# Performance work log

Measured on AMD Instinct MI355X. Metric: run time of the kernel, lower is better.

Reference implementation:

```python
import jax, jax.numpy as jnp
import numpy as np

N = 100000   # nodes
E = 1600000  # edges (avg degree 16)
D = 128      # in = hidden = out channels
DROP_P = 0.2


def setup_inputs() -> dict:
    key = jax.random.key(0)
    ks = jax.random.split(key, 11)
    s = 1.0 / np.sqrt(D)  # glorot-ish scale
    inp = {
        "features": jax.random.normal(ks[0], (N, D), jnp.float32),
        "edge_index": jax.random.randint(ks[1], (2, E), 0, N, dtype=jnp.int64),
    }
    for i in range(3):
        inp[f"Wl{i}"] = jax.random.normal(ks[2 + 3 * i], (D, D), jnp.float32) * s
        inp[f"Wr{i}"] = jax.random.normal(ks[3 + 3 * i], (D, D), jnp.float32) * s
        inp[f"b{i}"] = jnp.zeros((D,), jnp.float32)
    return inp


def _sage_conv(x, src, dst, Wl, Wr, b):
    # PyG SAGEConv (aggr='max'): out = lin_l(max_{j->i} x_j) + lin_r(x_i)
    agg = jax.ops.segment_max(x[src], dst, num_segments=N)  # [N, D_in]
    agg = jnp.where(jnp.isfinite(agg), agg, 0.0)  # isolated nodes -> 0 (torch_scatter zero-init)
    return agg @ Wl + x @ Wr + b


def _dropout(x, key, p=DROP_P):
    keep = jax.random.bernoulli(key, 1.0 - p, x.shape)
    return jnp.where(keep, x / (1.0 - p), 0.0)


def reference(features, edge_index, Wl0, Wr0, b0, Wl1, Wr1, b1, Wl2, Wr2, b2):
    src, dst = edge_index[0], edge_index[1]
    k1, k2 = jax.random.split(jax.random.key(42))
    x = _sage_conv(features, src, dst, Wl0, Wr0, b0)
    x = _dropout(jax.nn.elu(x), k1)
    x = _sage_conv(x, src, dst, Wl1, Wr1, b1)
    x = _dropout(jax.nn.elu(x), k2)
    x = _sage_conv(x, src, dst, Wl2, Wr2, b2)
    return x
```

## Files before the change

kernel.cpp:

```cpp
#include <hip/hip_runtime.h>
#include <math.h>

#define D 128
#define BSHIFT 9
#define BCAP 12288

typedef __attribute__((ext_vector_type(8))) _Float16 half8;
typedef __attribute__((ext_vector_type(4))) float floatx4;

__host__ __device__ __forceinline__ unsigned rotl32(unsigned v, int r) {
  return (v << r) | (v >> (32 - r));
}

__host__ __device__ __forceinline__ void threefry2x32(unsigned k0, unsigned k1,
                                                      unsigned x0, unsigned x1,
                                                      unsigned &o0, unsigned &o1) {
  unsigned ks2 = k0 ^ k1 ^ 0x1BD11BDAu;
  unsigned v0 = x0 + k0;
  unsigned v1 = x1 + k1;
  v0 += v1; v1 = rotl32(v1, 13); v1 ^= v0;
  v0 += v1; v1 = rotl32(v1, 15); v1 ^= v0;
  v0 += v1; v1 = rotl32(v1, 26); v1 ^= v0;
  v0 += v1; v1 = rotl32(v1, 6);  v1 ^= v0;
  v0 += k1; v1 += ks2 + 1u;
  v0 += v1; v1 = rotl32(v1, 17); v1 ^= v0;
  v0 += v1; v1 = rotl32(v1, 29); v1 ^= v0;
  v0 += v1; v1 = rotl32(v1, 16); v1 ^= v0;
  v0 += v1; v1 = rotl32(v1, 24); v1 ^= v0;
  v0 += ks2; v1 += k0 + 2u;
  v0 += v1; v1 = rotl32(v1, 13); v1 ^= v0;
  v0 += v1; v1 = rotl32(v1, 15); v1 ^= v0;
  v0 += v1; v1 = rotl32(v1, 26); v1 ^= v0;
  v0 += v1; v1 = rotl32(v1, 6);  v1 ^= v0;
  v0 += k0; v1 += k1 + 3u;
  v0 += v1; v1 = rotl32(v1, 17); v1 ^= v0;
  v0 += v1; v1 = rotl32(v1, 29); v1 ^= v0;
  v0 += v1; v1 = rotl32(v1, 16); v1 ^= v0;
  v0 += v1; v1 = rotl32(v1, 24); v1 ^= v0;
  v0 += k1; v1 += ks2 + 4u;
  v0 += v1; v1 = rotl32(v1, 13); v1 ^= v0;
  v0 += v1; v1 = rotl32(v1, 15); v1 ^= v0;
  v0 += v1; v1 = rotl32(v1, 26); v1 ^= v0;
  v0 += v1; v1 = rotl32(v1, 6);  v1 ^= v0;
  v0 += ks2; v1 += k0 + 5u;
  o0 = v0; o1 = v1;
}

__device__ __forceinline__ unsigned short f2h(float f) {
  _Float16 h = (_Float16)f;
  return *(unsigned short*)&h;
}

__device__ __forceinline__ unsigned pkmax(unsigned a, unsigned b) {
  unsigned r;
  asm("v_pk_max_f16 %0, %1, %2" : "=v"(r) : "v"(a), "v"(b));
  return r;
}


__global__ __launch_bounds__(256) void bucket_count_kernel(
    const int* __restrict__ dst, int* __restrict__ bucketTotal, int nEdges) {
  __shared__ int lc[256];
  int t = threadIdx.x;
  lc[t] = 0;
  __syncthreads();
  int e0 = blockIdx.x * 4096;
  for (int i = t; i < 4096; i += 256) {
    int e = e0 + i;
    if (e < nEdges) atomicAdd(&lc[dst[e] >> BSHIFT], 1);
  }
  __syncthreads();
  int c = lc[t];
  if (c > 0) atomicAdd(&bucketTotal[t], c);
}

__global__ __launch_bounds__(256) void scan_buckets_kernel(
    const int* __restrict__ bucketTotal, int* __restrict__ buckOff,
    int* __restrict__ bucketCursor, int nBuck) {
  __shared__ int s[256];
  int t = threadIdx.x;
  int v = (t < nBuck) ? bucketTotal[t] : 0;
  s[t] = v;
  __syncthreads();
  for (int off = 1; off < 256; off <<= 1) {
    int u = (t >= off) ? s[t - off] : 0;
    __syncthreads();
    s[t] += u;
    __syncthreads();
  }
  int excl = s[t] - v;
  if (t < nBuck) {
    buckOff[t] = excl;
    bucketCursor[t] = excl;
  } else if (t == nBuck) {
    buckOff[t] = s[255];
  }
}

__global__ __launch_bounds__(256) void bucket_scatter_kernel(
    const int* __restrict__ src, const int* __restrict__ dst,
    int* __restrict__ bucketCursor, unsigned* __restrict__ pairs,
    int nEdges, int nBuck) {
  __shared__ int lcount[256];
  __shared__ int lbase[256];
  __shared__ int loff[256];
  int t = threadIdx.x;
  lcount[t] = 0; loff[t] = 0;
  __syncthreads();
  int e0 = blockIdx.x * 4096;
  for (int i = t; i < 4096; i += 256) {
    int e = e0 + i;
    if (e < nEdges) atomicAdd(&lcount[dst[e] >> BSHIFT], 1);
  }
  __syncthreads();
  if (t < nBuck) {
    int c = lcount[t];
    if (c > 0) lbase[t] = atomicAdd(&bucketCursor[t], c);
  }
  __syncthreads();
  for (int i = t; i < 4096; i += 256) {
    int e = e0 + i;
    if (e < nEdges) {
      int d = dst[e];
      int b = d >> BSHIFT;
      int lp = atomicAdd(&loff[b], 1);
      pairs[lbase[b] + lp] = ((unsigned)src[e] << BSHIFT) | ((unsigned)d & 511u);
    }
  }
}

__global__ __launch_bounds__(256) void local_fill_kernel(
    const unsigned* __restrict__ pairs, const int* __restrict__ buckOff,
    int* __restrict__ rowStart, int* __restrict__ csrSrc,
    int nNodes, int nBuck) {
  __shared__ int sData[BCAP];
  __shared__ int lcnt[1 << BSHIFT];
  __shared__ int sSum[256];
  int b = blockIdx.x;
  int node0 = b << BSHIFT;
  int base = buckOff[b];
  int end = buckOff[b + 1];
  int cnt = end - base;
  int t = threadIdx.x;

  lcnt[t] = 0;
  lcnt[t + 256] = 0;
  __syncthreads();

  for (int i = base + t; i < end; i += 256)
    atomicAdd(&lcnt[pairs[i] & 511u], 1);
  __syncthreads();

  int c0 = lcnt[2 * t];
  int c1 = lcnt[2 * t + 1];
  int local = c0 + c1;
  sSum[t] = local;
  __syncthreads();
  for (int off = 1; off < 256; off <<= 1) {
    int v = (t >= off) ? sSum[t - off] : 0;
    __syncthreads();
    sSum[t] += v;
    __syncthreads();
  }
  int excl = sSum[t] - local;
  __syncthreads();
  lcnt[2 * t] = excl;
  lcnt[2 * t + 1] = excl + c0;
  int n0 = node0 + 2 * t;
  int n1 = n0 + 1;
  if (n0 < nNodes) rowStart[n0] = base + excl;
  if (n1 < nNodes) rowStart[n1] = base + excl + c0;
  if (b == nBuck - 1 && t == 255) rowStart[nNodes] = end;
  __syncthreads();

  if (cnt <= BCAP) {
    for (int i = base + t; i < end; i += 256) {
      unsigned p = pairs[i];
      int lp = atomicAdd(&lcnt[p & 511u], 1);
      sData[lp] = (int)(p >> BSHIFT);
    }
    __syncthreads();
    for (int i = t; i < cnt; i += 256)
      csrSrc[base + i] = sData[i];
  } else {
    for (int i = base + t; i < end; i += 256) {
      unsigned p = pairs[i];
      int lp = atomicAdd(&lcnt[p & 511u], 1);
      csrSrc[base + lp] = (int)(p >> BSHIFT);
    }
  }
}

__global__ __launch_bounds__(256) void convert_feat_kernel(
    const float* __restrict__ f, unsigned short* __restrict__ o, int nElems) {
  int i = (blockIdx.x * 256 + threadIdx.x) * 4;
  if (i + 3 < nElems) {
    float4 v = *((const float4*)(f + i));
    unsigned a = (unsigned)f2h(v.x) | ((unsigned)f2h(v.y) << 16);
    unsigned b = (unsigned)f2h(v.z) | ((unsigned)f2h(v.w) << 16);
    *((uint2*)(o + i)) = make_uint2(a, b);
  } else {
    for (int j = i; j < nElems; ++j) o[j] = f2h(f[j]);
  }
}

__global__ __launch_bounds__(256) void pack_weights_kernel(
    const float* __restrict__ Wl0, const float* __restrict__ Wr0,
    const float* __restrict__ Wl1, const float* __restrict__ Wr1,
    const float* __restrict__ Wl2, const float* __restrict__ Wr2,
    unsigned short* __restrict__ Wt) {
  int t = blockIdx.x * 256 + threadIdx.x;
  if (t >= 3 * 128 * 256) return;
  int l = t >> 15;
  int rem = t & 32767;
  int n = rem >> 8;
  int k = rem & 255;
  const float* Wl = (l == 0) ? Wl0 : (l == 1) ? Wl1 : Wl2;
  const float* Wr = (l == 0) ? Wr0 : (l == 1) ? Wr1 : Wr2;
  float v = (k < 128) ? Wl[k * D + n] : Wr[(k - 128) * D + n];
  Wt[t] = f2h(v);
}

__global__ __launch_bounds__(256) void gather_max_f16_kernel(
    const uint4* __restrict__ x8, const int* __restrict__ rowStart,
    const int* __restrict__ csrSrc, uint4* __restrict__ agg8, int nNodes) {
  int n = blockIdx.x * 4 + (threadIdx.x >> 6);
  if (n >= nNodes) return;
  int lane = threadIdx.x & 63;
  int q = lane >> 4;
  int l16 = lane & 15;
  int e0 = rowStart[n], e1 = rowStart[n + 1];
  unsigned m0 = 0xFC00FC00u, m1 = 0xFC00FC00u,
           m2 = 0xFC00FC00u, m3 = 0xFC00FC00u;
  int e = e0;
  for (; e + 15 < e1; e += 16) {
    int sa = csrSrc[e + q];
    int sb = csrSrc[e + 4 + q];
    int sc = csrSrc[e + 8 + q];
    int sd = csrSrc[e + 12 + q];
    uint4 va = x8[(size_t)sa * 16 + l16];
    uint4 vb = x8[(size_t)sb * 16 + l16];
    uint4 vc = x8[(size_t)sc * 16 + l16];
    uint4 vd = x8[(size_t)sd * 16 + l16];
    m0 = pkmax(m0, pkmax(pkmax(va.x, vb.x), pkmax(vc.x, vd.x)));
    m1 = pkmax(m1, pkmax(pkmax(va.y, vb.y), pkmax(vc.y, vd.y)));
    m2 = pkmax(m2, pkmax(pkmax(va.z, vb.z), pkmax(vc.z, vd.z)));
    m3 = pkmax(m3, pkmax(pkmax(va.w, vb.w), pkmax(vc.w, vd.w)));
  }
  if (e + 7 < e1) {
    int sa = csrSrc[e + q];
    int sb = csrSrc[e + 4 + q];
    uint4 va = x8[(size_t)sa * 16 + l16];
    uint4 vb = x8[(size_t)sb * 16 + l16];
    m0 = pkmax(m0, pkmax(va.x, vb.x));
    m1 = pkmax(m1, pkmax(va.y, vb.y));
    m2 = pkmax(m2, pkmax(va.z, vb.z));
    m3 = pkmax(m3, pkmax(va.w, vb.w));
    e += 8;
  }
  if (e + 3 < e1) {
    int sa = csrSrc[e + q];
    uint4 va = x8[(size_t)sa * 16 + l16];
    m0 = pkmax(m0, va.x); m1 = pkmax(m1, va.y);
    m2 = pkmax(m2, va.z); m3 = pkmax(m3, va.w);
    e += 4;
  }
  for (; e < e1; ++e) {
    int sa = csrSrc[e];
    uint4 va = x8[(size_t)sa * 16 + l16];
    m0 = pkmax(m0, va.x); m1 = pkmax(m1, va.y);
    m2 = pkmax(m2, va.z); m3 = pkmax(m3, va.w);
  }
  m0 = pkmax(m0, (unsigned)__shfl_xor((int)m0, 16, 64));
  m1 = pkmax(m1, (unsigned)__shfl_xor((int)m1, 16, 64));
  m2 = pkmax(m2, (unsigned)__shfl_xor((int)m2, 16, 64));
  m3 = pkmax(m3, (unsigned)__shfl_xor((int)m3, 16, 64));
  m0 = pkmax(m0, (unsigned)__shfl_xor((int)m0, 32, 64));
  m1 = pkmax(m1, (unsigned)__shfl_xor((int)m1, 32, 64));
  m2 = pkmax(m2, (unsigned)__shfl_xor((int)m2, 32, 64));
  m3 = pkmax(m3, (unsigned)__shfl_xor((int)m3, 32, 64));
  uint4 r = make_uint4(0u, 0u, 0u, 0u);
  if (e0 != e1) r = make_uint4(m0, m1, m2, m3);
  if (q == 0) agg8[(size_t)n * 16 + l16] = r;
}

#define PA 280
#define TROWS 64

__global__ __launch_bounds__(256, 2) void fused_mfma_kernel(
    const unsigned short* __restrict__ agghf, unsigned short* __restrict__ xhf,
    const unsigned short* __restrict__ Wt, const float* __restrict__ bias,
    float* __restrict__ outF, int nRows, int mode, unsigned kk0, unsigned kk1) {
  __shared__ unsigned short sA[TROWS * PA];

  const int tid = threadIdx.x;
  const int row0 = blockIdx.x * TROWS;
  const int wv = tid >> 6, lane = tid & 63;
  const int quad = lane >> 4, m16 = lane & 15;
  const int nbase = wv * 32;

#pragma unroll
  for (int i = 0; i < 8; ++i) {
    int idx = i * 256 + tid;
    int r = idx >> 5;
    int seg = idx & 31;
    uint4 v = make_uint4(0, 0, 0, 0);
    if (row0 + r < nRows) {
      if (seg < 16) v = ((const uint4*)(agghf + (size_t)(row0 + r) * D))[seg];
      else          v = ((const uint4*)(xhf  + (size_t)(row0 + r) * D))[seg - 16];
    }
    *((uint4*)(sA + r * PA + seg * 8)) = v;
  }

  half8 bfr[2][4][2];
#pragma unroll
  for (int kc = 0; kc < 2; ++kc)
#pragma unroll
    for (int ks = 0; ks < 4; ++ks)
#pragma unroll
      for (int j = 0; j < 2; ++j)
        bfr[kc][ks][j] = *((const half8*)(
            Wt + (size_t)(nbase + j * 16 + m16) * 256 + kc * 128 + ks * 32 + quad * 8));

  unsigned dmask = 0u;
  if (mode < 2) {
#pragma unroll
    for (int j = 0; j < 2; ++j) {
      int col = nbase + j * 16 + m16;
#pragma unroll
      for (int i = 0; i < 4; ++i) {
#pragma unroll
        for (int reg = 0; reg < 4; ++reg) {
          int r = row0 + i * 16 + quad * 4 + reg;
          unsigned jj = (unsigned)r * D + col;
          unsigned y0, y1;
          threefry2x32(kk0, kk1, 0u, jj, y0, y1);
          float u = __uint_as_float((((y0 ^ y1) >> 9)) | 0x3F800000u) - 1.0f;
          if (u < 0.8f) dmask |= (1u << (j * 16 + i * 4 + reg));
        }
      }
    }
  }

  floatx4 acc[4][2];
#pragma unroll
  for (int i = 0; i < 4; ++i)
#pragma unroll
    for (int j = 0; j < 2; ++j) acc[i][j] = (floatx4)(0.0f);

  __syncthreads();

#pragma unroll
  for (int kc = 0; kc < 2; ++kc)
#pragma unroll
    for (int ks = 0; ks < 4; ++ks) {
      int kA = kc * 128 + ks * 32 + quad * 8;
#pragma unroll
      for (int i = 0; i < 4; ++i) {
        half8 a = *((const half8*)(sA + (m16 + 16 * i) * PA + kA));
        acc[i][0] = __builtin_amdgcn_mfma_f32_16x16x32_f16(a, bfr[kc][ks][0], acc[i][0], 0, 0, 0);
        acc[i][1] = __builtin_amdgcn_mfma_f32_16x16x32_f16(a, bfr[kc][ks][1], acc[i][1], 0, 0, 0);
      }
    }

  if (mode < 2) {
    __syncthreads();
#pragma unroll
    for (int j = 0; j < 2; ++j) {
      int col = nbase + j * 16 + m16;
      float bc = bias[col];
#pragma unroll
      for (int i = 0; i < 4; ++i) {
#pragma unroll
        for (int reg = 0; reg < 4; ++reg) {
          int r = i * 16 + quad * 4 + reg;
          if (row0 + r >= nRows) continue;
          float v = acc[i][j][reg] + bc;
          v = (v > 0.0f) ? v : (__expf(v) - 1.0f);
          v = ((dmask >> (j * 16 + i * 4 + reg)) & 1u) ? v * 1.25f : 0.0f;
          sA[r * PA + col] = f2h(v);
        }
      }
    }
    __syncthreads();
#pragma unroll
    for (int i = 0; i < 4; ++i) {
      int idx = i * 256 + tid;
      int r = idx >> 4;
      int seg = idx & 15;
      if (row0 + r < nRows)
        ((uint4*)xhf)[(size_t)(row0 + r) * 16 + seg] =
            *((const uint4*)(sA + r * PA + seg * 8));
    }
  } else {
#pragma unroll
    for (int j = 0; j < 2; ++j) {
      int col = nbase + j * 16 + m16;
      float bc = bias[col];
#pragma unroll
      for (int i = 0; i < 4; ++i) {
#pragma unroll
        for (int reg = 0; reg < 4; ++reg) {
          int r = row0 + i * 16 + quad * 4 + reg;
          if (r >= nRows) continue;
          outF[(size_t)r * D + col] = acc[i][j][reg] + bc;
        }
      }
    }
  }
}

extern "C" void kernel_launch(void* const* d_in, const int* in_sizes, int n_in,
                              void* d_out, int out_size, void* d_ws, size_t ws_size,
                              hipStream_t stream) {
  const float* feat = (const float*)d_in[0];
  const int* ei = (const int*)d_in[1];
  const float* Wl0 = (const float*)d_in[2];
  const float* Wr0 = (const float*)d_in[3];
  const float* b0 = (const float*)d_in[4];
  const float* Wl1 = (const float*)d_in[5];
  const float* Wr1 = (const float*)d_in[6];
  const float* b1 = (const float*)d_in[7];
  const float* Wl2 = (const float*)d_in[8];
  const float* Wr2 = (const float*)d_in[9];
  const float* b2 = (const float*)d_in[10];

  const int N = in_sizes[0] / D;
  const int E = in_sizes[1] / 2;
  const int* src = ei;
  const int* dst = ei + E;

  const size_t hfBytes = (size_t)N * D * 2;
  char* wsp = (char*)d_ws;
  size_t off = 0;
  unsigned short* xhf   = (unsigned short*)(wsp + off); off += hfBytes;
  unsigned short* agghf = (unsigned short*)(wsp + off); off += hfBytes;
  unsigned short* Wt    = (unsigned short*)(wsp + off); off += ((size_t)3 * 128 * 256 * 2 + 511) & ~511ull;
  int* rowStart     = (int*)(wsp + off); off += ((size_t)(N + 1) * 4 + 511) & ~511ull;
  int* bucketTotal  = (int*)(wsp + off); off += 2048;
  int* buckOff      = (int*)(wsp + off); off += 2048;
  int* bucketCursor = (int*)(wsp + off); off += 2048;
  int* csrSrc    = (int*)(wsp + off); off += (size_t)E * 4;
  unsigned* pairs = (unsigned*)(wsp + off); off += (size_t)E * 4;

  const int nBuck = (N + (1 << BSHIFT) - 1) >> BSHIFT;

  unsigned k1a, k1b, k2a, k2b;
  threefry2x32(0u, 42u, 0u, 0u, k1a, k1b);
  threefry2x32(0u, 42u, 0u, 1u, k2a, k2b);

  hipMemsetAsync(bucketTotal, 0, 1024, stream);
  bucket_count_kernel<<<(E + 4095) / 4096, 256, 0, stream>>>(dst, bucketTotal, E);
  scan_buckets_kernel<<<1, 256, 0, stream>>>(bucketTotal, buckOff, bucketCursor, nBuck);
  bucket_scatter_kernel<<<(E + 4095) / 4096, 256, 0, stream>>>(src, dst, bucketCursor, pairs, E, nBuck);
  local_fill_kernel<<<nBuck, 256, 0, stream>>>(pairs, buckOff, rowStart, csrSrc, N, nBuck);

  convert_feat_kernel<<<(N * D / 4 + 255) / 256, 256, 0, stream>>>(feat, xhf, N * D);
  pack_weights_kernel<<<(3 * 128 * 256 + 255) / 256, 256, 0, stream>>>(
      Wl0, Wr0, Wl1, Wr1, Wl2, Wr2, Wt);

  dim3 blk(256);
  dim3 grdMax((N + 3) / 4);
  dim3 grdGemm((N + TROWS - 1) / TROWS);
  float* outF = (float*)d_out;

  gather_max_f16_kernel<<<grdMax, blk, 0, stream>>>((const uint4*)xhf, rowStart, csrSrc, (uint4*)agghf, N);
  fused_mfma_kernel<<<grdGemm, blk, 0, stream>>>(agghf, xhf, Wt, b0, outF, N, 0, k1a, k1b);

  gather_max_f16_kernel<<<grdMax, blk, 0, stream>>>((const uint4*)xhf, rowStart, csrSrc, (uint4*)agghf, N);
  fused_mfma_kernel<<<grdGemm, blk, 0, stream>>>(agghf, xhf, Wt + 32768, b1, outF, N, 1, k2a, k2b);

  gather_max_f16_kernel<<<grdMax, blk, 0, stream>>>((const uint4*)xhf, rowStart, csrSrc, (uint4*)agghf, N);
  fused_mfma_kernel<<<grdGemm, blk, 0, stream>>>(agghf, xhf, Wt + 65536, b2, outF, N, 2, 0u, 0u);
}
```

Measured before the change: 483.3 us.

## Merge prep kernels into one launch and shrink GEMM tile to 48 rows

Feature conversion, weight packing and bucket counting now run as block ranges of a single prep kernel, which removes two launches and lets these independent jobs overlap. The fused MFMA kernel drops from 64 to 48 rows per block, with launch bounds raised to 5 blocks per CU, so each block uses less LDS and more blocks stay resident to hide the latency of staging and the epilogue. In exchange each block reloads the same weight fragments over fewer rows, and the dropout mask bit packing is reindexed to match the smaller tile.

```diff
diff --git a/kernel.cpp b/kernel.cpp
--- a/kernel.cpp
+++ b/kernel.cpp
@@ -57,21 +57,51 @@
   return r;
 }
 
-
-__global__ __launch_bounds__(256) void bucket_count_kernel(
-    const int* __restrict__ dst, int* __restrict__ bucketTotal, int nEdges) {
-  __shared__ int lc[256];
+__global__ __launch_bounds__(256) void prep_kernel(
+    const float* __restrict__ feat, unsigned short* __restrict__ xhf,
+    const float* __restrict__ Wl0, const float* __restrict__ Wr0,
+    const float* __restrict__ Wl1, const float* __restrict__ Wr1,
+    const float* __restrict__ Wl2, const float* __restrict__ Wr2,
+    unsigned short* __restrict__ Wt,
+    const int* __restrict__ dst, int* __restrict__ bucketTotal,
+    int nElems, int nEdges, int nConv, int nPack) {
+  int b = blockIdx.x;
   int t = threadIdx.x;
-  lc[t] = 0;
-  __syncthreads();
-  int e0 = blockIdx.x * 4096;
-  for (int i = t; i < 4096; i += 256) {
-    int e = e0 + i;
-    if (e < nEdges) atomicAdd(&lc[dst[e] >> BSHIFT], 1);
-  }
-  __syncthreads();
-  int c = lc[t];
-  if (c > 0) atomicAdd(&bucketTotal[t], c);
+  if (b < nConv) {
+    int i = (b * 256 + t) * 4;
+    if (i + 3 < nElems) {
+      float4 v = *((const float4*)(feat + i));
+      unsigned a = (unsigned)f2h(v.x) | ((unsigned)f2h(v.y) << 16);
+      unsigned c = (unsigned)f2h(v.z) | ((unsigned)f2h(v.w) << 16);
+      *((uint2*)(xhf + i)) = make_uint2(a, c);
+    } else {
+      for (int j = i; j < nElems; ++j) xhf[j] = f2h(feat[j]);
+    }
+  } else if (b < nConv + nPack) {
+    int w = (b - nConv) * 256 + t;
+    if (w < 3 * 128 * 256) {
+      int l = w >> 15;
+      int rem = w & 32767;
+      int n = rem >> 8;
+      int k = rem & 255;
+      const float* Wl = (l == 0) ? Wl0 : (l == 1) ? Wl1 : Wl2;
+      const float* Wr = (l == 0) ? Wr0 : (l == 1) ? Wr1 : Wr2;
+      float v = (k < 128) ? Wl[k * D + n] : Wr[(k - 128) * D + n];
+      Wt[w] = f2h(v);
+    }
+  } else {
+    __shared__ int lc[256];
+    lc[t] = 0;
+    __syncthreads();
+    int e0 = (b - nConv - nPack) * 4096;
+    for (int i = t; i < 4096; i += 256) {
+      int e = e0 + i;
+      if (e < nEdges) atomicAdd(&lc[dst[e] >> BSHIFT], 1);
+    }
+    __syncthreads();
+    int c = lc[t];
+    if (c > 0) atomicAdd(&bucketTotal[t], c);
+  }
 }
 
 __global__ __launch_bounds__(256) void scan_buckets_kernel(
@@ -189,36 +219,6 @@
       csrSrc[base + lp] = (int)(p >> BSHIFT);
     }
   }
-}
-
-__global__ __launch_bounds__(256) void convert_feat_kernel(
-    const float* __restrict__ f, unsigned short* __restrict__ o, int nElems) {
-  int i = (blockIdx.x * 256 + threadIdx.x) * 4;
-  if (i + 3 < nElems) {
-    float4 v = *((const float4*)(f + i));
-    unsigned a = (unsigned)f2h(v.x) | ((unsigned)f2h(v.y) << 16);
-    unsigned b = (unsigned)f2h(v.z) | ((unsigned)f2h(v.w) << 16);
-    *((uint2*)(o + i)) = make_uint2(a, b);
-  } else {
-    for (int j = i; j < nElems; ++j) o[j] = f2h(f[j]);
-  }
-}
-
-__global__ __launch_bounds__(256) void pack_weights_kernel(
-    const float* __restrict__ Wl0, const float* __restrict__ Wr0,
-    const float* __restrict__ Wl1, const float* __restrict__ Wr1,
-    const float* __restrict__ Wl2, const float* __restrict__ Wr2,
-    unsigned short* __restrict__ Wt) {
-  int t = blockIdx.x * 256 + threadIdx.x;
-  if (t >= 3 * 128 * 256) return;
-  int l = t >> 15;
-  int rem = t & 32767;
-  int n = rem >> 8;
-  int k = rem & 255;
-  const float* Wl = (l == 0) ? Wl0 : (l == 1) ? Wl1 : Wl2;
-  const float* Wr = (l == 0) ? Wr0 : (l == 1) ? Wr1 : Wr2;
-  float v = (k < 128) ? Wl[k * D + n] : Wr[(k - 128) * D + n];
-  Wt[t] = f2h(v);
 }
 
 __global__ __launch_bounds__(256) void gather_max_f16_kernel(
@@ -285,9 +285,9 @@
 }
 
 #define PA 280
-#define TROWS 64
-
-__global__ __launch_bounds__(256, 2) void fused_mfma_kernel(
+#define TROWS 48
+
+__global__ __launch_bounds__(256, 5) void fused_mfma_kernel(
     const unsigned short* __restrict__ agghf, unsigned short* __restrict__ xhf,
     const unsigned short* __restrict__ Wt, const float* __restrict__ bias,
     float* __restrict__ outF, int nRows, int mode, unsigned kk0, unsigned kk1) {
@@ -300,7 +300,7 @@
   const int nbase = wv * 32;
 
 #pragma unroll
-  for (int i = 0; i < 8; ++i) {
+  for (int i = 0; i < 6; ++i) {
     int idx = i * 256 + tid;
     int r = idx >> 5;
     int seg = idx & 31;
@@ -328,7 +328,7 @@
     for (int j = 0; j < 2; ++j) {
       int col = nbase + j * 16 + m16;
 #pragma unroll
-      for (int i = 0; i < 4; ++i) {
+      for (int i = 0; i < 3; ++i) {
 #pragma unroll
         for (int reg = 0; reg < 4; ++reg) {
           int r = row0 + i * 16 + quad * 4 + reg;
@@ -336,15 +336,15 @@
           unsigned y0, y1;
           threefry2x32(kk0, kk1, 0u, jj, y0, y1);
           float u = __uint_as_float((((y0 ^ y1) >> 9)) | 0x3F800000u) - 1.0f;
-          if (u < 0.8f) dmask |= (1u << (j * 16 + i * 4 + reg));
+          if (u < 0.8f) dmask |= (1u << (j * 12 + i * 4 + reg));
         }
       }
     }
   }
 
-  floatx4 acc[4][2];
-#pragma unroll
-  for (int i = 0; i < 4; ++i)
+  floatx4 acc[3][2];
+#pragma unroll
+  for (int i = 0; i < 3; ++i)
 #pragma unroll
     for (int j = 0; j < 2; ++j) acc[i][j] = (floatx4)(0.0f);
 
@@ -356,7 +356,7 @@
     for (int ks = 0; ks < 4; ++ks) {
       int kA = kc * 128 + ks * 32 + quad * 8;
 #pragma unroll
-      for (int i = 0; i < 4; ++i) {
+      for (int i = 0; i < 3; ++i) {
         half8 a = *((const half8*)(sA + (m16 + 16 * i) * PA + kA));
         acc[i][0] = __builtin_amdgcn_mfma_f32_16x16x32_f16(a, bfr[kc][ks][0], acc[i][0], 0, 0, 0);
         acc[i][1] = __builtin_amdgcn_mfma_f32_16x16x32_f16(a, bfr[kc][ks][1], acc[i][1], 0, 0, 0);
@@ -370,21 +370,21 @@
       int col = nbase + j * 16 + m16;
       float bc = bias[col];
 #pragma unroll
-      for (int i = 0; i < 4; ++i) {
+      for (int i = 0; i < 3; ++i) {
 #pragma unroll
         for (int reg = 0; reg < 4; ++reg) {
           int r = i * 16 + quad * 4 + reg;
           if (row0 + r >= nRows) continue;
           float v = acc[i][j][reg] + bc;
           v = (v > 0.0f) ? v : (__expf(v) - 1.0f);
-          v = ((dmask >> (j * 16 + i * 4 + reg)) & 1u) ? v * 1.25f : 0.0f;
+          v = ((dmask >> (j * 12 + i * 4 + reg)) & 1u) ? v * 1.25f : 0.0f;
           sA[r * PA + col] = f2h(v);
         }
       }
     }
     __syncthreads();
 #pragma unroll
-    for (int i = 0; i < 4; ++i) {
+    for (int i = 0; i < 3; ++i) {
       int idx = i * 256 + tid;
       int r = idx >> 4;
       int seg = idx & 15;
@@ -398,7 +398,7 @@
       int col = nbase + j * 16 + m16;
       float bc = bias[col];
 #pragma unroll
-      for (int i = 0; i < 4; ++i) {
+      for (int i = 0; i < 3; ++i) {
 #pragma unroll
         for (int reg = 0; reg < 4; ++reg) {
           int r = row0 + i * 16 + quad * 4 + reg;
@@ -449,15 +449,16 @@
   threefry2x32(0u, 42u, 0u, 0u, k1a, k1b);
   threefry2x32(0u, 42u, 0u, 1u, k2a, k2b);
 
+  const int nConv = (N * D / 4 + 255) / 256;
+  const int nPack = (3 * 128 * 256 + 255) / 256;
+  const int nCount = (E + 4095) / 4096;
   hipMemsetAsync(bucketTotal, 0, 1024, stream);
-  bucket_count_kernel<<<(E + 4095) / 4096, 256, 0, stream>>>(dst, bucketTotal, E);
+  prep_kernel<<<nConv + nPack + nCount, 256, 0, stream>>>(
+      feat, xhf, Wl0, Wr0, Wl1, Wr1, Wl2, Wr2, Wt,
+      dst, bucketTotal, N * D, E, nConv, nPack);
   scan_buckets_kernel<<<1, 256, 0, stream>>>(bucketTotal, buckOff, bucketCursor, nBuck);
   bucket_scatter_kernel<<<(E + 4095) / 4096, 256, 0, stream>>>(src, dst, bucketCursor, pairs, E, nBuck);
   local_fill_kernel<<<nBuck, 256, 0, stream>>>(pairs, buckOff, rowStart, csrSrc, N, nBuck);
-
-  convert_feat_kernel<<<(N * D / 4 + 255) / 256, 256, 0, stream>>>(feat, xhf, N * D);
-  pack_weights_kernel<<<(3 * 128 * 256 + 255) / 256, 256, 0, stream>>>(
-      Wl0, Wr0, Wl1, Wr1, Wl2, Wr2, Wt);
 
   dim3 blk(256);
   dim3 grdMax((N + 3) / 4);
```

Measured after the change: 482.1 us. Within noise of the previous version (-0.2%).
